# Kernel optimization log

Measured on AMD Instinct MI355X. Metric: run time of the kernel, lower is better.

Reference implementation:

```python
import jax, jax.numpy as jnp
import numpy as np
from jax import lax

T, H, I, E = 1024, 2048, 1024, 16
G, TOPK_GROUP, TOP_K = 4, 2, 4
ROUTED_SCALE = 2.5
W_SCALE = 0.02  # keep activations in a sane range


def setup_inputs() -> dict:
    key = jax.random.key(0)
    ks = jax.random.split(key, 7)
    return {
        "hidden_states": jax.random.normal(ks[0], (T, H), jnp.float32),
        "gate_w": jax.random.normal(ks[1], (E, H), jnp.float32) * W_SCALE,
        "e_bias": jax.random.normal(ks[2], (E,), jnp.float32),
        "w_gate_up": jax.random.normal(ks[3], (E, 2 * I, H), jnp.float32) * W_SCALE,
        "w_down": jax.random.normal(ks[4], (E, H, I), jnp.float32) * W_SCALE,
        "shared_w_gate_up": jax.random.normal(ks[5], (2 * I, H), jnp.float32) * W_SCALE,
        "shared_w_down": jax.random.normal(ks[6], (H, I), jnp.float32) * W_SCALE,
    }


def _grouped_topk(scores, e_bias):
    # scores: sigmoid router scores [T, E]
    scores_b = scores + e_bias[None, :]
    # group score = sum of top-2 biased scores within each group (bias branch)
    group_scores = jnp.sum(lax.top_k(scores_b.reshape(-1, G, E // G), 2)[0], axis=-1)  # [T, G]
    _, group_idx = lax.top_k(group_scores, TOPK_GROUP)  # [T, topk_group]
    group_mask = jnp.any(jax.nn.one_hot(group_idx, G, dtype=jnp.bool_), axis=1)  # [T, G]
    score_mask = jnp.repeat(group_mask, E // G, axis=-1)  # [T, E]
    tmp = jnp.where(score_mask, scores_b, 0.0)
    _, topk_ids = lax.top_k(tmp, TOP_K)  # [T, K]
    topk_w = jnp.take_along_axis(scores, topk_ids, axis=1)  # weights from UNbiased scores
    topk_w = topk_w / jnp.sum(topk_w, axis=-1, keepdims=True)  # renormalize
    return topk_w, topk_ids


def _silu_and_mul(gu):
    g, u = jnp.split(gu, 2, axis=-1)
    return jax.nn.silu(g) * u


def reference(hidden_states, gate_w, e_bias, w_gate_up, w_down,
              shared_w_gate_up, shared_w_down):
    x = hidden_states  # [T, H]
    # shared expert MLP
    shared = _silu_and_mul(x @ shared_w_gate_up.T) @ shared_w_down.T  # [T, H]
    # router
    logits = x @ gate_w.T                      # [T, E]
    scores = jax.nn.sigmoid(logits)
    topk_w, topk_ids = _grouped_topk(scores, e_bias)
    # dense combine weights [T, E] (zero for unselected experts)
    combine = jnp.zeros((T, E), x.dtype).at[jnp.arange(T)[:, None], topk_ids].add(topk_w)
    # routed experts: SwiGLU per expert, combined with routing weights
    gu = jnp.einsum('th,eih->tei', x, w_gate_up)        # [T, E, 2I]
    a = _silu_and_mul(gu)                               # [T, E, I]
    routed = jnp.einsum('tei,ehi,te->th', a, w_down, combine)  # [T, H]
    return routed * ROUTED_SCALE + shared
```

## Files before the change

kernel.cpp:

```cpp
#include <hip/hip_runtime.h>
#include <math.h>

typedef __bf16 bf16;
typedef bf16 bf16x4 __attribute__((ext_vector_type(4)));
typedef bf16 bf16x8 __attribute__((ext_vector_type(8)));
typedef float f32x4 __attribute__((ext_vector_type(4)));

#define T_TOK   1024
#define H_DIM   2048
#define I_DIM   1024
#define E_NUM   16
#define NPAIR_R 4096
#define NPAIR   5120
#define LDSS    40

__global__ __launch_bounds__(256) void router_kernel(
    const float* __restrict__ x, const float* __restrict__ gate_w,
    const float* __restrict__ e_bias,
    int* __restrict__ topk_ids, float* __restrict__ topk_w,
    int* __restrict__ counts)
{
  int t = blockIdx.x;
  int tid = threadIdx.x;
  float acc[16];
#pragma unroll
  for (int e = 0; e < 16; ++e) acc[e] = 0.f;
  const float* xr = x + (size_t)t * H_DIM;
  for (int h = tid; h < H_DIM; h += 256) {
    float xv = xr[h];
#pragma unroll
    for (int e = 0; e < 16; ++e) acc[e] += xv * gate_w[e * H_DIM + h];
  }
#pragma unroll
  for (int e = 0; e < 16; ++e) {
#pragma unroll
    for (int off = 32; off >= 1; off >>= 1)
      acc[e] += __shfl_down(acc[e], off, 64);
  }
  __shared__ float red[4][16];
  int lane = tid & 63, wave = tid >> 6;
  if (lane == 0) {
#pragma unroll
    for (int e = 0; e < 16; ++e) red[wave][e] = acc[e];
  }
  __syncthreads();
  if (tid == 0) {
    float scores[16], sb[16];
    for (int e = 0; e < 16; ++e) {
      float l = red[0][e] + red[1][e] + red[2][e] + red[3][e];
      float s = 1.f / (1.f + expf(-l));
      scores[e] = s;
      sb[e] = s + e_bias[e];
    }
    float gs[4];
    for (int g = 0; g < 4; ++g) {
      float b1 = -1e30f, b2 = -1e30f;
      for (int j = 0; j < 4; ++j) {
        float v = sb[g * 4 + j];
        if (v > b1) { b2 = b1; b1 = v; }
        else if (v > b2) b2 = v;
      }
      gs[g] = b1 + b2;
    }
    int g1 = 0; float bv = gs[0];
    for (int g = 1; g < 4; ++g) if (gs[g] > bv) { bv = gs[g]; g1 = g; }
    int g2 = -1; float bv2 = -1e30f;
    for (int g = 0; g < 4; ++g) if (g != g1 && gs[g] > bv2) { bv2 = gs[g]; g2 = g; }
    float tmp[16];
    for (int e = 0; e < 16; ++e) {
      int grp = e >> 2;
      tmp[e] = (grp == g1 || grp == g2) ? sb[e] : 0.0f;
    }
    bool used[16] = {false};
    int ids[4]; float wv[4]; float wsum = 0.f;
    for (int k = 0; k < 4; ++k) {
      int bi = 0; float bvv = -1e30f;
      for (int i = 0; i < 16; ++i)
        if (!used[i] && tmp[i] > bvv) { bvv = tmp[i]; bi = i; }
      used[bi] = true;
      ids[k] = bi; wv[k] = scores[bi]; wsum += scores[bi];
    }
    float inv = 1.f / wsum;
    for (int k = 0; k < 4; ++k) {
      topk_ids[t * 4 + k] = ids[k];
      topk_w[t * 4 + k] = wv[k] * inv;
      atomicAdd(&counts[ids[k]], 1);
    }
  }
}

__global__ void offsets_kernel(const int* __restrict__ counts, int* __restrict__ off)
{
  if (threadIdx.x == 0 && blockIdx.x == 0) {
    int s = 0;
    for (int e = 0; e < 16; ++e) { off[e] = s; s += counts[e]; }
    off[16] = s;
  }
}

__global__ __launch_bounds__(256) void scatter_kernel(
    const int* __restrict__ topk_ids, const float* __restrict__ topk_w,
    const int* __restrict__ off, int* __restrict__ cursor,
    int* __restrict__ pair_token, float* __restrict__ pair_scale)
{
  int i = blockIdx.x * 256 + threadIdx.x;
  if (i < NPAIR_R) {
    int e = topk_ids[i];
    float w = topk_w[i];
    int pos = atomicAdd(&cursor[e], 1);
    int idx = off[e] + pos;
    pair_token[idx] = i >> 2;
    pair_scale[idx] = 2.5f * w;
  } else if (i < NPAIR) {
    pair_token[i] = i - NPAIR_R;
    pair_scale[i] = 1.0f;
  }
}

__global__ __launch_bounds__(256) void gateup_kernel(
    const float* __restrict__ x, const float* __restrict__ w_gu,
    const float* __restrict__ s_wgu,
    const int* __restrict__ off, const int* __restrict__ pair_token,
    bf16* __restrict__ gu_buf)
{
  const int nt = blockIdx.x;
  const int mt = blockIdx.y;
  const int e  = blockIdx.z;
  const int poff = (e < 16) ? off[e]     : NPAIR_R;
  const int pend = (e < 16) ? off[e + 1] : NPAIR;
  const int cnt  = pend - poff;
  if (mt * 128 >= cnt) return;
  const float* __restrict__ B = (e < 16) ? (w_gu + (size_t)e * 2 * I_DIM * H_DIM) : s_wgu;

  __shared__ bf16 As[128 * LDSS];
  __shared__ bf16 Bs[128 * LDSS];

  const int tid = threadIdx.x;
  const int lane = tid & 63, wave = tid >> 6;
  const int wm = wave >> 1, wn = wave & 1;
  const int srow = tid >> 1;
  const int scol = (tid & 1) * 16;

  int rloc = mt * 128 + srow;
  int p_eff = poff + (rloc < cnt ? rloc : cnt - 1);
  const float* __restrict__ Arow = x + (size_t)pair_token[p_eff] * H_DIM;
  const float* __restrict__ Brow = B + (size_t)(nt * 128 + srow) * H_DIM;

  f32x4 acc[4][4];
  f32x4 zz = {0.f, 0.f, 0.f, 0.f};
#pragma unroll
  for (int mi = 0; mi < 4; ++mi)
#pragma unroll
    for (int ni = 0; ni < 4; ++ni) acc[mi][ni] = zz;

  for (int k0 = 0; k0 < H_DIM; k0 += 32) {
#pragma unroll
    for (int i = 0; i < 4; ++i) {
      float4 av = *(const float4*)(Arow + k0 + scol + 4 * i);
      float4 bv = *(const float4*)(Brow + k0 + scol + 4 * i);
      bf16x4 a4, b4;
      a4[0] = (bf16)av.x; a4[1] = (bf16)av.y; a4[2] = (bf16)av.z; a4[3] = (bf16)av.w;
      b4[0] = (bf16)bv.x; b4[1] = (bf16)bv.y; b4[2] = (bf16)bv.z; b4[3] = (bf16)bv.w;
      *(bf16x4*)(&As[srow * LDSS + scol + 4 * i]) = a4;
      *(bf16x4*)(&Bs[srow * LDSS + scol + 4 * i]) = b4;
    }
    __syncthreads();
    const int kq = (lane >> 4) * 8;
    bf16x8 af[4], bfv[4];
#pragma unroll
    for (int mi = 0; mi < 4; ++mi)
      af[mi] = *(const bf16x8*)(&As[(wm * 64 + mi * 16 + (lane & 15)) * LDSS + kq]);
#pragma unroll
    for (int ni = 0; ni < 4; ++ni)
      bfv[ni] = *(const bf16x8*)(&Bs[(wn * 64 + ni * 16 + (lane & 15)) * LDSS + kq]);
#pragma unroll
    for (int mi = 0; mi < 4; ++mi)
#pragma unroll
      for (int ni = 0; ni < 4; ++ni)
        acc[mi][ni] = __builtin_amdgcn_mfma_f32_16x16x32_bf16(af[mi], bfv[ni], acc[mi][ni], 0, 0, 0);
    __syncthreads();
  }

  const int colb = nt * 128 + wn * 64;
#pragma unroll
  for (int mi = 0; mi < 4; ++mi) {
#pragma unroll
    for (int reg = 0; reg < 4; ++reg) {
      int r = wm * 64 + mi * 16 + ((lane >> 4) * 4) + reg;
      int rl = mt * 128 + r;
      if (rl < cnt) {
        size_t p = (size_t)(poff + rl);
        bf16* orow = gu_buf + p * (2 * I_DIM) + colb + (lane & 15);
#pragma unroll
        for (int ni = 0; ni < 4; ++ni)
          orow[ni * 16] = (bf16)acc[mi][ni][reg];
      }
    }
  }
}

__global__ __launch_bounds__(256) void silu_kernel(
    const bf16* __restrict__ gu, bf16* __restrict__ a)
{
  int idx = (blockIdx.x * 256 + threadIdx.x) * 4;
  int p = idx >> 10;
  int c = idx & 1023;
  const bf16* g = gu + (size_t)p * (2 * I_DIM) + c;
  bf16x4 g4 = *(const bf16x4*)(g);
  bf16x4 u4 = *(const bf16x4*)(g + I_DIM);
  bf16x4 r;
#pragma unroll
  for (int j = 0; j < 4; ++j) {
    float gf = (float)g4[j];
    float uf = (float)u4[j];
    float s = gf / (1.f + expf(-gf));
    r[j] = (bf16)(s * uf);
  }
  *(bf16x4*)(a + idx) = r;
}

__global__ __launch_bounds__(256) void down_kernel(
    const bf16* __restrict__ a_buf, const float* __restrict__ w_dn,
    const float* __restrict__ s_wdn,
    const int* __restrict__ off, const int* __restrict__ pair_token,
    const float* __restrict__ pair_scale, float* __restrict__ out)
{
  const int nt = blockIdx.x;
  const int mt = blockIdx.y;
  const int e  = blockIdx.z;
  const int poff = (e < 16) ? off[e]     : NPAIR_R;
  const int pend = (e < 16) ? off[e + 1] : NPAIR;
  const int cnt  = pend - poff;
  if (mt * 128 >= cnt) return;
  const float* __restrict__ B = (e < 16) ? (w_dn + (size_t)e * H_DIM * I_DIM) : s_wdn;

  __shared__ bf16 As[128 * LDSS];
  __shared__ bf16 Bs[128 * LDSS];

  const int tid = threadIdx.x;
  const int lane = tid & 63, wave = tid >> 6;
  const int wm = wave >> 1, wn = wave & 1;
  const int srow = tid >> 1;
  const int scol = (tid & 1) * 16;

  const bf16* __restrict__ Arow = a_buf + (size_t)(poff + mt * 128 + srow) * I_DIM;
  const float* __restrict__ Brow = B + (size_t)(nt * 128 + srow) * I_DIM;

  f32x4 acc[4][4];
  f32x4 zz = {0.f, 0.f, 0.f, 0.f};
#pragma unroll
  for (int mi = 0; mi < 4; ++mi)
#pragma unroll
    for (int ni = 0; ni < 4; ++ni) acc[mi][ni] = zz;

  for (int k0 = 0; k0 < I_DIM; k0 += 32) {
    bf16x8 a0 = *(const bf16x8*)(Arow + k0 + scol);
    bf16x8 a1 = *(const bf16x8*)(Arow + k0 + scol + 8);
    *(bf16x8*)(&As[srow * LDSS + scol])     = a0;
    *(bf16x8*)(&As[srow * LDSS + scol + 8]) = a1;
#pragma unroll
    for (int i = 0; i < 4; ++i) {
      float4 bv = *(const float4*)(Brow + k0 + scol + 4 * i);
      bf16x4 b4;
      b4[0] = (bf16)bv.x; b4[1] = (bf16)bv.y; b4[2] = (bf16)bv.z; b4[3] = (bf16)bv.w;
      *(bf16x4*)(&Bs[srow * LDSS + scol + 4 * i]) = b4;
    }
    __syncthreads();
    const int kq = (lane >> 4) * 8;
    bf16x8 af[4], bfv[4];
#pragma unroll
    for (int mi = 0; mi < 4; ++mi)
      af[mi] = *(const bf16x8*)(&As[(wm * 64 + mi * 16 + (lane & 15)) * LDSS + kq]);
#pragma unroll
    for (int ni = 0; ni < 4; ++ni)
      bfv[ni] = *(const bf16x8*)(&Bs[(wn * 64 + ni * 16 + (lane & 15)) * LDSS + kq]);
#pragma unroll
    for (int mi = 0; mi < 4; ++mi)
#pragma unroll
      for (int ni = 0; ni < 4; ++ni)
        acc[mi][ni] = __builtin_amdgcn_mfma_f32_16x16x32_bf16(af[mi], bfv[ni], acc[mi][ni], 0, 0, 0);
    __syncthreads();
  }

  const int colb = nt * 128 + wn * 64;
#pragma unroll
  for (int mi = 0; mi < 4; ++mi) {
#pragma unroll
    for (int reg = 0; reg < 4; ++reg) {
      int r = wm * 64 + mi * 16 + ((lane >> 4) * 4) + reg;
      int rl = mt * 128 + r;
      if (rl < cnt) {
        int p = poff + rl;
        int tok = pair_token[p];
        float sc = pair_scale[p];
        float* orow = out + (size_t)tok * H_DIM + colb + (lane & 15);
#pragma unroll
        for (int ni = 0; ni < 4; ++ni)
          atomicAdd(&orow[ni * 16], acc[mi][ni][reg] * sc);
      }
    }
  }
}

extern "C" void kernel_launch(void* const* d_in, const int* in_sizes, int n_in,
                              void* d_out, int out_size, void* d_ws, size_t ws_size,
                              hipStream_t stream)
{
  const float* x     = (const float*)d_in[0];
  const float* gatew = (const float*)d_in[1];
  const float* ebias = (const float*)d_in[2];
  const float* w_gu  = (const float*)d_in[3];
  const float* w_dn  = (const float*)d_in[4];
  const float* s_wgu = (const float*)d_in[5];
  const float* s_wdn = (const float*)d_in[6];
  float* out = (float*)d_out;

  char* ws = (char*)d_ws;
  int*   off        = (int*)(ws + 0);
  int*   counts     = (int*)(ws + 128);
  int*   cursor     = (int*)(ws + 192);
  int*   topk_ids   = (int*)(ws + 256);
  float* topk_w     = (float*)(ws + 16640);
  int*   pair_token = (int*)(ws + 33024);
  float* pair_scale = (float*)(ws + 53504);
  bf16*  gu_buf     = (bf16*)(ws + 73984);
  bf16*  a_buf      = (bf16*)(ws + 73984 + 20971520);

  hipMemsetAsync(out, 0, (size_t)T_TOK * H_DIM * sizeof(float), stream);
  hipMemsetAsync(ws + 128, 0, 128, stream);

  router_kernel<<<T_TOK, 256, 0, stream>>>(x, gatew, ebias, topk_ids, topk_w, counts);
  offsets_kernel<<<1, 64, 0, stream>>>(counts, off);
  scatter_kernel<<<NPAIR / 256, 256, 0, stream>>>(topk_ids, topk_w, off, cursor,
                                                  pair_token, pair_scale);
  dim3 g1(16, 8, 17);
  gateup_kernel<<<g1, 256, 0, stream>>>(x, w_gu, s_wgu, off, pair_token, gu_buf);
  silu_kernel<<<(NPAIR * I_DIM) / (256 * 4), 256, 0, stream>>>(gu_buf, a_buf);
  dim3 g2(16, 8, 17);
  down_kernel<<<g2, 256, 0, stream>>>(a_buf, w_dn, s_wdn, off, pair_token, pair_scale, out);
}
```

Baseline: 665.8 us.

## Fuse SiLU into gate-up GEMM, double-buffer LDS, replace atomics with combine pass

The gate-up GEMM now loads matching gate and up rows into one tile and applies SiLU-and-multiply in its epilogue. This removes the intermediate gate-up buffer and the separate silu kernel. Both GEMMs use a register-prefetched double-buffered LDS pipeline, so each k-step needs one barrier instead of two. The down GEMM writes scaled bf16 partials per pair, and a new combine kernel sums each token's five partials through an inverse pair map, which removes the output memset and the fp32 atomics. In exchange, partial sums are rounded to bf16, and the extra combine pass reads a bf16 partials buffer of 5120 by 2048 entries.

```diff
diff --git a/kernel.cpp b/kernel.cpp
--- a/kernel.cpp
+++ b/kernel.cpp
@@ -9,10 +9,20 @@
 #define T_TOK   1024
 #define H_DIM   2048
 #define I_DIM   1024
-#define E_NUM   16
 #define NPAIR_R 4096
 #define NPAIR   5120
+#define BK      32
 #define LDSS    40
+#define ABUF    10240
+#define BUFSZ   20480
+#define SMEM_SZ 40960
+
+__device__ inline bf16x8 cvt8(const float4 a, const float4 b) {
+  bf16x8 r;
+  r[0] = (bf16)a.x; r[1] = (bf16)a.y; r[2] = (bf16)a.z; r[3] = (bf16)a.w;
+  r[4] = (bf16)b.x; r[5] = (bf16)b.y; r[6] = (bf16)b.z; r[7] = (bf16)b.w;
+  return r;
+}
 
 __global__ __launch_bounds__(256) void router_kernel(
     const float* __restrict__ x, const float* __restrict__ gate_w,
@@ -101,7 +111,8 @@
 __global__ __launch_bounds__(256) void scatter_kernel(
     const int* __restrict__ topk_ids, const float* __restrict__ topk_w,
     const int* __restrict__ off, int* __restrict__ cursor,
-    int* __restrict__ pair_token, float* __restrict__ pair_scale)
+    int* __restrict__ pair_token, float* __restrict__ pair_scale,
+    int* __restrict__ inv_pair)
 {
   int i = blockIdx.x * 256 + threadIdx.x;
   if (i < NPAIR_R) {
@@ -109,19 +120,23 @@
     float w = topk_w[i];
     int pos = atomicAdd(&cursor[e], 1);
     int idx = off[e] + pos;
-    pair_token[idx] = i >> 2;
+    int t = i >> 2;
+    pair_token[idx] = t;
     pair_scale[idx] = 2.5f * w;
+    inv_pair[t * 5 + (i & 3)] = idx;
   } else if (i < NPAIR) {
-    pair_token[i] = i - NPAIR_R;
+    int t = i - NPAIR_R;
+    pair_token[i] = t;
     pair_scale[i] = 1.0f;
-  }
-}
-
-__global__ __launch_bounds__(256) void gateup_kernel(
+    inv_pair[t * 5 + 4] = i;
+  }
+}
+
+__global__ __launch_bounds__(256) void gateup_silu_kernel(
     const float* __restrict__ x, const float* __restrict__ w_gu,
     const float* __restrict__ s_wgu,
     const int* __restrict__ off, const int* __restrict__ pair_token,
-    bf16* __restrict__ gu_buf)
+    bf16* __restrict__ a_buf)
 {
   const int nt = blockIdx.x;
   const int mt = blockIdx.y;
@@ -132,98 +147,121 @@
   if (mt * 128 >= cnt) return;
   const float* __restrict__ B = (e < 16) ? (w_gu + (size_t)e * 2 * I_DIM * H_DIM) : s_wgu;
 
-  __shared__ bf16 As[128 * LDSS];
-  __shared__ bf16 Bs[128 * LDSS];
+  __shared__ char smem[SMEM_SZ];
 
   const int tid = threadIdx.x;
   const int lane = tid & 63, wave = tid >> 6;
   const int wm = wave >> 1, wn = wave & 1;
   const int srow = tid >> 1;
   const int scol = (tid & 1) * 16;
+  const int l15 = lane & 15;
+  const int kq = (lane >> 4) * 8;
 
   int rloc = mt * 128 + srow;
   int p_eff = poff + (rloc < cnt ? rloc : cnt - 1);
-  const float* __restrict__ Arow = x + (size_t)pair_token[p_eff] * H_DIM;
-  const float* __restrict__ Brow = B + (size_t)(nt * 128 + srow) * H_DIM;
+  const float* __restrict__ Arow = x + (size_t)pair_token[p_eff] * H_DIM + scol;
+  int brow_g = nt * 64 + (srow < 64 ? srow : 960 + srow);
+  const float* __restrict__ Brow = B + (size_t)brow_g * H_DIM + scol;
 
   f32x4 acc[4][4];
-  f32x4 zz = {0.f, 0.f, 0.f, 0.f};
 #pragma unroll
   for (int mi = 0; mi < 4; ++mi)
 #pragma unroll
-    for (int ni = 0; ni < 4; ++ni) acc[mi][ni] = zz;
-
-  for (int k0 = 0; k0 < H_DIM; k0 += 32) {
-#pragma unroll
-    for (int i = 0; i < 4; ++i) {
-      float4 av = *(const float4*)(Arow + k0 + scol + 4 * i);
-      float4 bv = *(const float4*)(Brow + k0 + scol + 4 * i);
-      bf16x4 a4, b4;
-      a4[0] = (bf16)av.x; a4[1] = (bf16)av.y; a4[2] = (bf16)av.z; a4[3] = (bf16)av.w;
-      b4[0] = (bf16)bv.x; b4[1] = (bf16)bv.y; b4[2] = (bf16)bv.z; b4[3] = (bf16)bv.w;
-      *(bf16x4*)(&As[srow * LDSS + scol + 4 * i]) = a4;
-      *(bf16x4*)(&Bs[srow * LDSS + scol + 4 * i]) = b4;
+    for (int ni = 0; ni < 4; ++ni) { acc[mi][ni][0]=0.f; acc[mi][ni][1]=0.f; acc[mi][ni][2]=0.f; acc[mi][ni][3]=0.f; }
+
+  float4 ar[4], br[4];
+#pragma unroll
+  for (int i = 0; i < 4; ++i) {
+    ar[i] = *(const float4*)(Arow + 4 * i);
+    br[i] = *(const float4*)(Brow + 4 * i);
+  }
+  {
+    bf16* As = (bf16*)(smem);
+    bf16* Bs = (bf16*)(smem + ABUF);
+    *(bf16x8*)(As + srow * LDSS + scol)     = cvt8(ar[0], ar[1]);
+    *(bf16x8*)(As + srow * LDSS + scol + 8) = cvt8(ar[2], ar[3]);
+    *(bf16x8*)(Bs + srow * LDSS + scol)     = cvt8(br[0], br[1]);
+    *(bf16x8*)(Bs + srow * LDSS + scol + 8) = cvt8(br[2], br[3]);
+  }
+  __syncthreads();
+  int cur = 0;
+  for (int k0 = BK; ; k0 += BK) {
+    const bool more = (k0 < H_DIM);
+    if (more) {
+#pragma unroll
+      for (int i = 0; i < 4; ++i) {
+        ar[i] = *(const float4*)(Arow + k0 + 4 * i);
+        br[i] = *(const float4*)(Brow + k0 + 4 * i);
+      }
+    }
+    {
+      const bf16* As = (const bf16*)(smem + cur * BUFSZ);
+      const bf16* Bs = (const bf16*)(smem + cur * BUFSZ + ABUF);
+      bf16x8 af[4], bfv[4];
+#pragma unroll
+      for (int mi = 0; mi < 4; ++mi)
+        af[mi] = *(const bf16x8*)(As + (wm * 64 + mi * 16 + l15) * LDSS + kq);
+#pragma unroll
+      for (int ni = 0; ni < 4; ++ni)
+        bfv[ni] = *(const bf16x8*)(Bs + (wn * 64 + ni * 16 + l15) * LDSS + kq);
+#pragma unroll
+      for (int mi = 0; mi < 4; ++mi)
+#pragma unroll
+        for (int ni = 0; ni < 4; ++ni)
+          acc[mi][ni] = __builtin_amdgcn_mfma_f32_16x16x32_bf16(af[mi], bfv[ni], acc[mi][ni], 0, 0, 0);
+    }
+    if (more) {
+      bf16* As = (bf16*)(smem + (cur ^ 1) * BUFSZ);
+      bf16* Bs = (bf16*)(smem + (cur ^ 1) * BUFSZ + ABUF);
+      *(bf16x8*)(As + srow * LDSS + scol)     = cvt8(ar[0], ar[1]);
+      *(bf16x8*)(As + srow * LDSS + scol + 8) = cvt8(ar[2], ar[3]);
+      *(bf16x8*)(Bs + srow * LDSS + scol)     = cvt8(br[0], br[1]);
+      *(bf16x8*)(Bs + srow * LDSS + scol + 8) = cvt8(br[2], br[3]);
     }
     __syncthreads();
-    const int kq = (lane >> 4) * 8;
-    bf16x8 af[4], bfv[4];
+    cur ^= 1;
+    if (!more) break;
+  }
+
+  float* u_lds = (float*)smem;
+  if (wn == 1) {
 #pragma unroll
     for (int mi = 0; mi < 4; ++mi)
-      af[mi] = *(const bf16x8*)(&As[(wm * 64 + mi * 16 + (lane & 15)) * LDSS + kq]);
-#pragma unroll
-    for (int ni = 0; ni < 4; ++ni)
-      bfv[ni] = *(const bf16x8*)(&Bs[(wn * 64 + ni * 16 + (lane & 15)) * LDSS + kq]);
+#pragma unroll
+      for (int reg = 0; reg < 4; ++reg) {
+        int r = wm * 64 + mi * 16 + (lane >> 4) * 4 + reg;
+#pragma unroll
+        for (int ni = 0; ni < 4; ++ni)
+          u_lds[r * 65 + ni * 16 + l15] = acc[mi][ni][reg];
+      }
+  }
+  __syncthreads();
+  if (wn == 0) {
 #pragma unroll
     for (int mi = 0; mi < 4; ++mi)
 #pragma unroll
-      for (int ni = 0; ni < 4; ++ni)
-        acc[mi][ni] = __builtin_amdgcn_mfma_f32_16x16x32_bf16(af[mi], bfv[ni], acc[mi][ni], 0, 0, 0);
-    __syncthreads();
-  }
-
-  const int colb = nt * 128 + wn * 64;
-#pragma unroll
-  for (int mi = 0; mi < 4; ++mi) {
-#pragma unroll
-    for (int reg = 0; reg < 4; ++reg) {
-      int r = wm * 64 + mi * 16 + ((lane >> 4) * 4) + reg;
-      int rl = mt * 128 + r;
-      if (rl < cnt) {
-        size_t p = (size_t)(poff + rl);
-        bf16* orow = gu_buf + p * (2 * I_DIM) + colb + (lane & 15);
-#pragma unroll
-        for (int ni = 0; ni < 4; ++ni)
-          orow[ni * 16] = (bf16)acc[mi][ni][reg];
+      for (int reg = 0; reg < 4; ++reg) {
+        int r = wm * 64 + mi * 16 + (lane >> 4) * 4 + reg;
+        int rl = mt * 128 + r;
+        if (rl < cnt) {
+          bf16* orow = a_buf + (size_t)(poff + rl) * I_DIM + nt * 64 + l15;
+#pragma unroll
+          for (int ni = 0; ni < 4; ++ni) {
+            float g = acc[mi][ni][reg];
+            float u = u_lds[r * 65 + ni * 16 + l15];
+            float s = g / (1.f + __expf(-g));
+            orow[ni * 16] = (bf16)(s * u);
+          }
+        }
       }
-    }
-  }
-}
-
-__global__ __launch_bounds__(256) void silu_kernel(
-    const bf16* __restrict__ gu, bf16* __restrict__ a)
-{
-  int idx = (blockIdx.x * 256 + threadIdx.x) * 4;
-  int p = idx >> 10;
-  int c = idx & 1023;
-  const bf16* g = gu + (size_t)p * (2 * I_DIM) + c;
-  bf16x4 g4 = *(const bf16x4*)(g);
-  bf16x4 u4 = *(const bf16x4*)(g + I_DIM);
-  bf16x4 r;
-#pragma unroll
-  for (int j = 0; j < 4; ++j) {
-    float gf = (float)g4[j];
-    float uf = (float)u4[j];
-    float s = gf / (1.f + expf(-gf));
-    r[j] = (bf16)(s * uf);
-  }
-  *(bf16x4*)(a + idx) = r;
+  }
 }
 
 __global__ __launch_bounds__(256) void down_kernel(
     const bf16* __restrict__ a_buf, const float* __restrict__ w_dn,
     const float* __restrict__ s_wdn,
-    const int* __restrict__ off, const int* __restrict__ pair_token,
-    const float* __restrict__ pair_scale, float* __restrict__ out)
+    const int* __restrict__ off, const float* __restrict__ pair_scale,
+    bf16* __restrict__ dpart)
 {
   const int nt = blockIdx.x;
   const int mt = blockIdx.y;
@@ -234,52 +272,77 @@
   if (mt * 128 >= cnt) return;
   const float* __restrict__ B = (e < 16) ? (w_dn + (size_t)e * H_DIM * I_DIM) : s_wdn;
 
-  __shared__ bf16 As[128 * LDSS];
-  __shared__ bf16 Bs[128 * LDSS];
+  __shared__ char smem[SMEM_SZ];
 
   const int tid = threadIdx.x;
   const int lane = tid & 63, wave = tid >> 6;
   const int wm = wave >> 1, wn = wave & 1;
   const int srow = tid >> 1;
   const int scol = (tid & 1) * 16;
-
-  const bf16* __restrict__ Arow = a_buf + (size_t)(poff + mt * 128 + srow) * I_DIM;
-  const float* __restrict__ Brow = B + (size_t)(nt * 128 + srow) * I_DIM;
+  const int l15 = lane & 15;
+  const int kq = (lane >> 4) * 8;
+
+  int rloc = mt * 128 + srow;
+  int r_eff = poff + (rloc < cnt ? rloc : cnt - 1);
+  const bf16* __restrict__ Arow = a_buf + (size_t)r_eff * I_DIM + scol;
+  const float* __restrict__ Brow = B + (size_t)(nt * 128 + srow) * I_DIM + scol;
 
   f32x4 acc[4][4];
-  f32x4 zz = {0.f, 0.f, 0.f, 0.f};
 #pragma unroll
   for (int mi = 0; mi < 4; ++mi)
 #pragma unroll
-    for (int ni = 0; ni < 4; ++ni) acc[mi][ni] = zz;
-
-  for (int k0 = 0; k0 < I_DIM; k0 += 32) {
-    bf16x8 a0 = *(const bf16x8*)(Arow + k0 + scol);
-    bf16x8 a1 = *(const bf16x8*)(Arow + k0 + scol + 8);
-    *(bf16x8*)(&As[srow * LDSS + scol])     = a0;
-    *(bf16x8*)(&As[srow * LDSS + scol + 8]) = a1;
-#pragma unroll
-    for (int i = 0; i < 4; ++i) {
-      float4 bv = *(const float4*)(Brow + k0 + scol + 4 * i);
-      bf16x4 b4;
-      b4[0] = (bf16)bv.x; b4[1] = (bf16)bv.y; b4[2] = (bf16)bv.z; b4[3] = (bf16)bv.w;
-      *(bf16x4*)(&Bs[srow * LDSS + scol + 4 * i]) = b4;
+    for (int ni = 0; ni < 4; ++ni) { acc[mi][ni][0]=0.f; acc[mi][ni][1]=0.f; acc[mi][ni][2]=0.f; acc[mi][ni][3]=0.f; }
+
+  bf16x8 a0, a1; float4 br[4];
+  a0 = *(const bf16x8*)(Arow);
+  a1 = *(const bf16x8*)(Arow + 8);
+#pragma unroll
+  for (int i = 0; i < 4; ++i) br[i] = *(const float4*)(Brow + 4 * i);
+  {
+    bf16* As = (bf16*)(smem);
+    bf16* Bs = (bf16*)(smem + ABUF);
+    *(bf16x8*)(As + srow * LDSS + scol)     = a0;
+    *(bf16x8*)(As + srow * LDSS + scol + 8) = a1;
+    *(bf16x8*)(Bs + srow * LDSS + scol)     = cvt8(br[0], br[1]);
+    *(bf16x8*)(Bs + srow * LDSS + scol + 8) = cvt8(br[2], br[3]);
+  }
+  __syncthreads();
+  int cur = 0;
+  for (int k0 = BK; ; k0 += BK) {
+    const bool more = (k0 < I_DIM);
+    if (more) {
+      a0 = *(const bf16x8*)(Arow + k0);
+      a1 = *(const bf16x8*)(Arow + k0 + 8);
+#pragma unroll
+      for (int i = 0; i < 4; ++i) br[i] = *(const float4*)(Brow + k0 + 4 * i);
+    }
+    {
+      const bf16* As = (const bf16*)(smem + cur * BUFSZ);
+      const bf16* Bs = (const bf16*)(smem + cur * BUFSZ + ABUF);
+      bf16x8 af[4], bfv[4];
+#pragma unroll
+      for (int mi = 0; mi < 4; ++mi)
+        af[mi] = *(const bf16x8*)(As + (wm * 64 + mi * 16 + l15) * LDSS + kq);
+#pragma unroll
+      for (int ni = 0; ni < 4; ++ni)
+        bfv[ni] = *(const bf16x8*)(Bs + (wn * 64 + ni * 16 + l15) * LDSS + kq);
+#pragma unroll
+      for (int mi = 0; mi < 4; ++mi)
+#pragma unroll
+        for (int ni = 0; ni < 4; ++ni)
+          acc[mi][ni] = __builtin_amdgcn_mfma_f32_16x16x32_bf16(af[mi], bfv[ni], acc[mi][ni], 0, 0, 0);
+    }
+    if (more) {
+      bf16* As = (bf16*)(smem + (cur ^ 1) * BUFSZ);
+      bf16* Bs = (bf16*)(smem + (cur ^ 1) * BUFSZ + ABUF);
+      *(bf16x8*)(As + srow * LDSS + scol)     = a0;
+      *(bf16x8*)(As + srow * LDSS + scol + 8) = a1;
+      *(bf16x8*)(Bs + srow * LDSS + scol)     = cvt8(br[0], br[1]);
+      *(bf16x8*)(Bs + srow * LDSS + scol + 8) = cvt8(br[2], br[3]);
     }
     __syncthreads();
-    const int kq = (lane >> 4) * 8;
-    bf16x8 af[4], bfv[4];
-#pragma unroll
-    for (int mi = 0; mi < 4; ++mi)
-      af[mi] = *(const bf16x8*)(&As[(wm * 64 + mi * 16 + (lane & 15)) * LDSS + kq]);
-#pragma unroll
-    for (int ni = 0; ni < 4; ++ni)
-      bfv[ni] = *(const bf16x8*)(&Bs[(wn * 64 + ni * 16 + (lane & 15)) * LDSS + kq]);
-#pragma unroll
-    for (int mi = 0; mi < 4; ++mi)
-#pragma unroll
-      for (int ni = 0; ni < 4; ++ni)
-        acc[mi][ni] = __builtin_amdgcn_mfma_f32_16x16x32_bf16(af[mi], bfv[ni], acc[mi][ni], 0, 0, 0);
-    __syncthreads();
+    cur ^= 1;
+    if (!more) break;
   }
 
   const int colb = nt * 128 + wn * 64;
@@ -287,19 +350,35 @@
   for (int mi = 0; mi < 4; ++mi) {
 #pragma unroll
     for (int reg = 0; reg < 4; ++reg) {
-      int r = wm * 64 + mi * 16 + ((lane >> 4) * 4) + reg;
+      int r = wm * 64 + mi * 16 + (lane >> 4) * 4 + reg;
       int rl = mt * 128 + r;
       if (rl < cnt) {
         int p = poff + rl;
-        int tok = pair_token[p];
         float sc = pair_scale[p];
-        float* orow = out + (size_t)tok * H_DIM + colb + (lane & 15);
+        bf16* orow = dpart + (size_t)p * H_DIM + colb + l15;
 #pragma unroll
         for (int ni = 0; ni < 4; ++ni)
-          atomicAdd(&orow[ni * 16], acc[mi][ni][reg] * sc);
+          orow[ni * 16] = (bf16)(acc[mi][ni][reg] * sc);
       }
     }
   }
+}
+
+__global__ __launch_bounds__(256) void combine_kernel(
+    const bf16* __restrict__ dpart, const int* __restrict__ inv_pair,
+    float* __restrict__ out)
+{
+  int i = (blockIdx.x * 256 + threadIdx.x) * 4;
+  int t = i >> 11;
+  int h = i & 2047;
+  const int* iv = inv_pair + t * 5;
+  float4 s = {0.f, 0.f, 0.f, 0.f};
+#pragma unroll
+  for (int j = 0; j < 5; ++j) {
+    bf16x4 d = *(const bf16x4*)(dpart + (size_t)iv[j] * H_DIM + h);
+    s.x += (float)d[0]; s.y += (float)d[1]; s.z += (float)d[2]; s.w += (float)d[3];
+  }
+  *(float4*)(out + i) = s;
 }
 
 extern "C" void kernel_launch(void* const* d_in, const int* in_sizes, int n_in,
@@ -323,19 +402,19 @@
   float* topk_w     = (float*)(ws + 16640);
   int*   pair_token = (int*)(ws + 33024);
   float* pair_scale = (float*)(ws + 53504);
-  bf16*  gu_buf     = (bf16*)(ws + 73984);
-  bf16*  a_buf      = (bf16*)(ws + 73984 + 20971520);
-
-  hipMemsetAsync(out, 0, (size_t)T_TOK * H_DIM * sizeof(float), stream);
+  int*   inv_pair   = (int*)(ws + 73984);
+  bf16*  a_buf      = (bf16*)(ws + 94464);
+  bf16*  dpart      = (bf16*)(ws + 10580224);
+
   hipMemsetAsync(ws + 128, 0, 128, stream);
 
   router_kernel<<<T_TOK, 256, 0, stream>>>(x, gatew, ebias, topk_ids, topk_w, counts);
   offsets_kernel<<<1, 64, 0, stream>>>(counts, off);
   scatter_kernel<<<NPAIR / 256, 256, 0, stream>>>(topk_ids, topk_w, off, cursor,
-                                                  pair_token, pair_scale);
+                                                  pair_token, pair_scale, inv_pair);
   dim3 g1(16, 8, 17);
-  gateup_kernel<<<g1, 256, 0, stream>>>(x, w_gu, s_wgu, off, pair_token, gu_buf);
-  silu_kernel<<<(NPAIR * I_DIM) / (256 * 4), 256, 0, stream>>>(gu_buf, a_buf);
+  gateup_silu_kernel<<<g1, 256, 0, stream>>>(x, w_gu, s_wgu, off, pair_token, a_buf);
   dim3 g2(16, 8, 17);
-  down_kernel<<<g2, 256, 0, stream>>>(a_buf, w_dn, s_wdn, off, pair_token, pair_scale, out);
-}
+  down_kernel<<<g2, 256, 0, stream>>>(a_buf, w_dn, s_wdn, off, pair_scale, dpart);
+  combine_kernel<<<(T_TOK * H_DIM) / (256 * 4), 256, 0, stream>>>(dpart, inv_pair, out);
+}
```

Result: slower. 688.2 us (+3.4%).
